# Kernel tuning notes

Hardware: AMD Instinct MI355X
Metric: run time of the kernel (lower is better)

The kernel has to match this reference:

```python
import jax, jax.numpy as jnp
import numpy as np

EMBED_DIM = 256
NUM_HEADS = 4
HEAD_DIM = EMBED_DIM // NUM_HEADS  # 64
FEAT_X = FEAT_Y = 64               # 64*64 = 4096 tokens
THETA = 10000.0


def _axial_cos_sin(dim, end_x, end_y, theta):
    # compute_axial_cis: dim//4 frequencies per spatial axis, concatenated -> [N, dim//2]
    f = 1.0 / (theta ** (np.arange(0, dim, 4)[: dim // 4].astype(np.float32) / dim))
    t = np.arange(end_x * end_y)
    tx = (t % end_x).astype(np.float32)
    ty = (t // end_x).astype(np.float32)
    ang = np.concatenate([np.outer(tx, f), np.outer(ty, f)], axis=-1)  # [N, dim//2]
    return jnp.asarray(np.cos(ang)), jnp.asarray(np.sin(ang))


def _apply_rope(x, cos, sin):
    # x: [B, H, N, D]; adjacent pairs (x[..., 2i], x[..., 2i+1]) are the complex parts
    xr = x.reshape(*x.shape[:-1], -1, 2)
    xa, xb = xr[..., 0], xr[..., 1]          # [B, H, N, D//2]
    oa = xa * cos - xb * sin                  # cos/sin: [N, D//2], broadcast
    ob = xa * sin + xb * cos
    return jnp.stack([oa, ob], axis=-1).reshape(x.shape)


def setup_inputs() -> dict:
    key = jax.random.key(0)
    ks = jax.random.split(key, 8)
    B, N, D = 1, FEAT_X * FEAT_Y, EMBED_DIM
    s = 0.02  # weight init scale
    return {
        "q": jax.random.normal(ks[0], (B, N, D), jnp.float32),
        "k": jax.random.normal(ks[1], (B, N, D), jnp.float32),
        "v": jax.random.normal(ks[2], (B, N, D), jnp.float32),
        "wq": jax.random.normal(ks[3], (D, D), jnp.float32) * s,
        "bq": jnp.zeros((D,), jnp.float32),
        "wk": jax.random.normal(ks[4], (D, D), jnp.float32) * s,
        "bk": jnp.zeros((D,), jnp.float32),
        "wv": jax.random.normal(ks[5], (D, D), jnp.float32) * s,
        "bv": jnp.zeros((D,), jnp.float32),
        "wo": jax.random.normal(ks[6], (D, D), jnp.float32) * s,
        "bo": jnp.zeros((D,), jnp.float32),
        "return_attn": 0,
        "num_k_exclude_rope": 0,
    }


def reference(q, k, v, wq, bq, wk, bk, wv, bv, wo, bo, return_attn, num_k_exclude_rope):
    B, Nq, D = q.shape
    H, hd = NUM_HEADS, HEAD_DIM
    # QKV projections (weights stored [in, out], equiv to torch Linear W.T)
    qp = (q @ wq + bq).reshape(B, Nq, H, hd).transpose(0, 2, 1, 3)   # [B,H,Nq,hd]
    kp = (k @ wk + bk).reshape(B, -1, H, hd).transpose(0, 2, 1, 3)   # [B,H,Nk,hd]
    vp = (v @ wv + bv).reshape(B, -1, H, hd).transpose(0, 2, 1, 3)
    # rotary encoding on q and the first (Nk - num_k_exclude_rope) keys
    cos, sin = _axial_cos_sin(hd, FEAT_X, FEAT_Y, THETA)
    qp = _apply_rope(qp, cos, sin)
    nkr = kp.shape[2] - num_k_exclude_rope  # static Python int
    if num_k_exclude_rope > 0:
        kp = jnp.concatenate([_apply_rope(kp[:, :, :nkr], cos, sin), kp[:, :, nkr:]], axis=2)
    else:
        kp = _apply_rope(kp, cos, sin)
    # SDPA (eval: dropout_p = 0)
    scale = 1.0 / jnp.sqrt(jnp.asarray(hd, qp.dtype))
    scores = jnp.einsum("bhqd,bhkd->bhqk", qp, kp) * scale
    attn = jax.nn.softmax(scores, axis=-1)
    out = jnp.einsum("bhqk,bhkd->bhqd", attn, vp)
    out = out.transpose(0, 2, 1, 3).reshape(B, Nq, D)
    out = out @ wo + bo
    if return_attn:
        return out, scores  # attn_weight = q @ k^T * scale (pre-softmax, as in source)
    return out
```

## Files before the change

kernel.cpp:

```cpp
#include <hip/hip_runtime.h>
#include <hip/hip_bf16.h>
#include <math.h>

#define NTOK 4096
#define DEMB 256
#define NHEAD 4
#define HD 64

typedef short bf16x8 __attribute__((ext_vector_type(8)));
typedef short bf16x4 __attribute__((ext_vector_type(4)));
typedef float f32x4 __attribute__((ext_vector_type(4)));

__device__ __forceinline__ unsigned short f2b(float f) {
  union { float f; unsigned u; } v; v.f = f;
  return (unsigned short)((v.u + 0x7FFFu + ((v.u >> 16) & 1u)) >> 16);
}
__device__ __forceinline__ unsigned packrp(float lo, float hi) {
  return __builtin_amdgcn_perm(__float_as_uint(hi) + 0x8000u,
                               __float_as_uint(lo) + 0x8000u, 0x07060302u);
}

__global__ void prep_kernel(const float* wq, const float* wk, const float* wv,
                            const float* wo, unsigned short* wt, float2* cs) {
  int b = blockIdx.x;
  if (b < 1024) {
    int idx = b * 256 + threadIdx.x;
    int m = idx >> 16, rest = idx & 0xFFFF;
    int o = rest >> 8, i = rest & 255;
    const float* w = (m == 0) ? wq : (m == 1) ? wk : (m == 2) ? wv : wo;
    wt[idx] = f2b(w[i * 256 + o]);
  } else {
    int idx = (b - 1024) * 256 + threadIdx.x;
    int n = idx >> 5, p = idx & 31;
    int j = p & 15;
    float f = powf(10000.0f, -(float)j / 16.0f);
    float ang = ((p < 16) ? (float)(n & 63) : (float)(n >> 6)) * f;
    cs[idx] = make_float2(cosf(ang), sinf(ang));
  }
}

__global__ __launch_bounds__(256) void qkvproj_kernel(
    const float* q, const float* k, const float* v, const unsigned short* wt,
    const float* bq, const float* bk, const float* bv, const float2* cs,
    unsigned short* qp, unsigned short* kp, unsigned short* vt) {
  int which = blockIdx.z;
  int wave = threadIdx.x >> 6, lane = threadIdx.x & 63;
  int col = lane & 15, g = lane >> 4;
  int mbase = blockIdx.x * 64 + wave * 16;
  int nbase = blockIdx.y * 64;
  const float* X = (which == 0) ? q : (which == 1) ? k : v;
  const unsigned short* W = wt + which * 65536;
  const float* bias = (which == 0) ? bq : (which == 1) ? bk : bv;

  f32x4 acc[4] = {};
  const float* ap0 = X + (mbase + col) * 256 + g * 8;
#pragma unroll
  for (int ks = 0; ks < 256; ks += 32) {
    float4 a0 = *(const float4*)(ap0 + ks);
    float4 a1 = *(const float4*)(ap0 + ks + 4);
    bf16x8 af;
    af[0] = (short)f2b(a0.x); af[1] = (short)f2b(a0.y);
    af[2] = (short)f2b(a0.z); af[3] = (short)f2b(a0.w);
    af[4] = (short)f2b(a1.x); af[5] = (short)f2b(a1.y);
    af[6] = (short)f2b(a1.z); af[7] = (short)f2b(a1.w);
#pragma unroll
    for (int nt = 0; nt < 4; ++nt) {
      bf16x8 bf_ = *(const bf16x8*)(W + (nbase + nt * 16 + col) * 256 + ks + g * 8);
      acc[nt] = __builtin_amdgcn_mfma_f32_16x16x32_bf16(af, bf_, acc[nt], 0, 0, 0);
    }
  }

  if (which == 2) {
    int kpos = ((mbase >> 5) << 5) + 8 * g + 4 * ((mbase >> 4) & 1);
#pragma unroll
    for (int nt = 0; nt < 4; ++nt) {
      int c = nbase + nt * 16 + col;
      float b = bias[c];
      bf16x4 pk;
#pragma unroll
      for (int r = 0; r < 4; ++r) pk[r] = (short)f2b(acc[nt][r] + b);
      *(bf16x4*)(vt + c * NTOK + kpos) = pk;
    }
  } else {
    const float QSC = 0.18033688f;
    unsigned short* dst = (which == 0) ? qp : kp;
#pragma unroll
    for (int nt = 0; nt < 4; ++nt) {
      int c = nbase + nt * 16 + col;
      float b = bias[c];
#pragma unroll
      for (int r = 0; r < 4; ++r) {
        int t = mbase + g * 4 + r;
        float val = acc[nt][r] + b;
        float2 csv = cs[t * 32 + ((c & 63) >> 1)];
        float pv = __shfl_xor(val, 1);
        float sn = (c & 1) ? csv.y : -csv.y;
        val = val * csv.x + pv * sn;
        if (which == 0) val *= QSC;
        dst[((c >> 6) * NTOK + t) * HD + (c & 63)] = f2b(val);
      }
    }
  }
}

__global__ __launch_bounds__(512, 4) void attn_kernel(
    const unsigned short* qp, const unsigned short* kp,
    const unsigned short* vt, float* pO, float* pml) {
  __shared__ alignas(16) unsigned char lds[32768];
  int id = blockIdx.x;
  int xcd = id & 7;
  int head = xcd >> 1;
  int rest = id >> 3;
  int qtile = rest >> 2;
  int ks = (xcd & 1) * 4 + (rest & 3);
  int qb = qtile * 128;
  int slot = (head * 32 + qtile) * 8 + ks;
  int w = threadIdx.x >> 6, lane = threadIdx.x & 63;
  int col = lane & 15, g = lane >> 4;
  int stok = threadIdx.x >> 3, spart = threadIdx.x & 7;
  unsigned soff = (unsigned)(stok * 128) +
                  (unsigned)((spart * 16) ^ ((stok & 7) << 4));

  const unsigned short* kgp = kp + (head * NTOK + ks * 512) * HD;
  const unsigned short* vgp = vt + head * HD * NTOK + ks * 512;

  bf16x8 skr, svr;
  auto stage_issue = [&](int t) {
    skr = *(const bf16x8*)(kgp + (t * 64 + stok) * HD + spart * 8);
    svr = *(const bf16x8*)(vgp + stok * NTOK + t * 64 + spart * 8);
  };
  auto stage_write = [&](int buf) {
    *(bf16x8*)(lds + (unsigned)buf * 16384u + soff) = skr;
    *(bf16x8*)(lds + (unsigned)buf * 16384u + 8192u + soff) = svr;
  };

  bf16x8 ones;
#pragma unroll
  for (int i = 0; i < 8; ++i) ones[i] = (short)0x3F80;

  bf16x8 qf[2];
  {
    const unsigned short* qr = qp + (head * NTOK + qb + w * 16) * HD;
#pragma unroll
    for (int h2 = 0; h2 < 2; ++h2)
      qf[h2] = *(const bf16x8*)(qr + col * HD + h2 * 32 + g * 8);
  }

  stage_issue(0);
  stage_write(0);
  stage_issue(1);
  __syncthreads();

  f32x4 acco[4] = {};
  f32x4 lacc = {};
  float mrow = -1e30f;

  for (int t = 0; t < 8; ++t) {
    int cur = t & 1;
    if (t < 7) {
      stage_write(cur ^ 1);
      if (t < 6) stage_issue(t + 2);
    }
    unsigned kb = (unsigned)cur * 16384u, vb = (unsigned)cur * 16384u + 8192u;

    f32x4 st[4] = {};
#pragma unroll
    for (int mt = 0; mt < 4; ++mt) {
      int tok = mt * 16 + col;
      unsigned ro = kb + (unsigned)(tok * 128) + (unsigned)((g * 16) ^ ((tok & 7) << 4));
      bf16x8 kf0 = *(const bf16x8*)(lds + ro);
      bf16x8 kf1 = *(const bf16x8*)(lds + (ro ^ 64u));
      st[mt] = __builtin_amdgcn_mfma_f32_16x16x32_bf16(kf0, qf[0], st[mt], 0, 0, 0);
      st[mt] = __builtin_amdgcn_mfma_f32_16x16x32_bf16(kf1, qf[1], st[mt], 0, 0, 0);
    }

    float pm = fmaxf(fmaxf(st[0][0], st[0][1]), fmaxf(st[0][2], st[0][3]));
#pragma unroll
    for (int mt = 1; mt < 4; ++mt)
      pm = fmaxf(pm, fmaxf(fmaxf(st[mt][0], st[mt][1]), fmaxf(st[mt][2], st[mt][3])));
    if (!__all(pm <= mrow + 8.0f)) {
      float nm = fmaxf(pm, __shfl_xor(pm, 16));
      nm = fmaxf(nm, __shfl_xor(nm, 32));
      nm = fmaxf(nm, mrow);
      float fac = exp2f(mrow - nm);
      mrow = nm;
      float fr0 = __shfl(fac, g * 4 + 0), fr1 = __shfl(fac, g * 4 + 1);
      float fr2 = __shfl(fac, g * 4 + 2), fr3 = __shfl(fac, g * 4 + 3);
#pragma unroll
      for (int nt = 0; nt < 4; ++nt) {
        acco[nt][0] *= fr0; acco[nt][1] *= fr1;
        acco[nt][2] *= fr2; acco[nt][3] *= fr3;
      }
      lacc[0] *= fr0; lacc[1] *= fr1; lacc[2] *= fr2; lacc[3] *= fr3;
    }

    float p[4][4];
#pragma unroll
    for (int mt = 0; mt < 4; ++mt)
#pragma unroll
      for (int r = 0; r < 4; ++r) p[mt][r] = exp2f(st[mt][r] - mrow);
    unsigned pw[2][4];
#pragma unroll
    for (int kk = 0; kk < 2; ++kk) {
      pw[kk][0] = packrp(p[2 * kk][0], p[2 * kk][1]);
      pw[kk][1] = packrp(p[2 * kk][2], p[2 * kk][3]);
      pw[kk][2] = packrp(p[2 * kk + 1][0], p[2 * kk + 1][1]);
      pw[kk][3] = packrp(p[2 * kk + 1][2], p[2 * kk + 1][3]);
    }

#pragma unroll
    for (int kk = 0; kk < 2; ++kk) {
      union { unsigned u[4]; bf16x8 v; } pf;
      pf.u[0] = pw[kk][0]; pf.u[1] = pw[kk][1];
      pf.u[2] = pw[kk][2]; pf.u[3] = pw[kk][3];
      lacc = __builtin_amdgcn_mfma_f32_16x16x32_bf16(pf.v, ones, lacc, 0, 0, 0);
#pragma unroll
      for (int nt = 0; nt < 4; ++nt) {
        int d = nt * 16 + col;
        unsigned off = vb + (unsigned)(d * 128) +
                       (unsigned)((kk * 64 + g * 16) ^ ((d & 7) << 4));
        bf16x8 vf = *(const bf16x8*)(lds + off);
        acco[nt] = __builtin_amdgcn_mfma_f32_16x16x32_bf16(pf.v, vf, acco[nt], 0, 0, 0);
      }
    }
    __syncthreads();
  }

#pragma unroll
  for (int nt = 0; nt < 4; ++nt)
#pragma unroll
    for (int r = 0; r < 4; ++r)
      pO[slot * 8192 + (w * 16 + g * 4 + r) * 64 + nt * 16 + col] = acco[nt][r];
  if (col == 0) {
#pragma unroll
    for (int r = 0; r < 4; ++r)
      pml[slot * 256 + (w * 16 + g * 4 + r) * 2 + 1] = lacc[r];
  }
  if (g == 0)
    pml[slot * 256 + (w * 16 + col) * 2 + 0] = mrow;
}

__global__ __launch_bounds__(256) void merge_kernel(
    const float* pO, const float* pml, unsigned short* att) {
  int bid = blockIdx.x;
  int group = bid >> 1, half = bid & 1;
  int head = group >> 5, qtile = group & 31;
  int t = threadIdx.x;
  int qloc = half * 64 + (t >> 2);
  int d0 = (t & 3) * 16;
  const float* mlb = pml + group * 8 * 256 + qloc * 2;
  float mx = -1e30f;
#pragma unroll
  for (int ks = 0; ks < 8; ++ks) mx = fmaxf(mx, mlb[ks * 256]);
  float den = 0.f, num[16] = {};
#pragma unroll
  for (int ks = 0; ks < 8; ++ks) {
    float wgt = exp2f(mlb[ks * 256] - mx);
    den += wgt * mlb[ks * 256 + 1];
    const float* ob = pO + (group * 8 + ks) * 8192 + qloc * 64 + d0;
#pragma unroll
    for (int i = 0; i < 16; ++i) num[i] += wgt * ob[i];
  }
  float inv = 1.0f / den;
  union { unsigned short s[16]; bf16x8 v[2]; } ov;
#pragma unroll
  for (int i = 0; i < 16; ++i) ov.s[i] = f2b(num[i] * inv);
  unsigned short* dst = att + (qtile * 128 + qloc) * DEMB + head * HD + d0;
  *(bf16x8*)dst = ov.v[0];
  *(bf16x8*)(dst + 8) = ov.v[1];
}

__global__ __launch_bounds__(256) void outproj_kernel(
    const unsigned short* att, const unsigned short* wt_o, const float* bo,
    float* out) {
  int wave = threadIdx.x >> 6, lane = threadIdx.x & 63;
  int col = lane & 15, g = lane >> 4;
  int mbase = blockIdx.x * 64 + wave * 16;
  int nbase = blockIdx.y * 64;
  f32x4 acc[4] = {};
#pragma unroll
  for (int ks = 0; ks < 256; ks += 32) {
    bf16x8 af = *(const bf16x8*)(att + (mbase + col) * 256 + ks + g * 8);
#pragma unroll
    for (int nt = 0; nt < 4; ++nt) {
      bf16x8 bf_ = *(const bf16x8*)(wt_o + (nbase + nt * 16 + col) * 256 + ks + g * 8);
      acc[nt] = __builtin_amdgcn_mfma_f32_16x16x32_bf16(af, bf_, acc[nt], 0, 0, 0);
    }
  }
#pragma unroll
  for (int nt = 0; nt < 4; ++nt) {
    int c = nbase + nt * 16 + col;
    float b = bo[c];
#pragma unroll
    for (int r = 0; r < 4; ++r)
      out[(mbase + g * 4 + r) * 256 + c] = acc[nt][r] + b;
  }
}

extern "C" void kernel_launch(void* const* d_in, const int* in_sizes, int n_in,
                              void* d_out, int out_size, void* d_ws, size_t ws_size,
                              hipStream_t stream) {
  const float* q  = (const float*)d_in[0];
  const float* k  = (const float*)d_in[1];
  const float* v  = (const float*)d_in[2];
  const float* wq = (const float*)d_in[3];
  const float* bq = (const float*)d_in[4];
  const float* wk = (const float*)d_in[5];
  const float* bk = (const float*)d_in[6];
  const float* wv = (const float*)d_in[7];
  const float* bv = (const float*)d_in[8];
  const float* wo = (const float*)d_in[9];
  const float* bo = (const float*)d_in[10];
  float* out = (float*)d_out;

  char* ws = (char*)d_ws;
  float2* cs         = (float2*)ws;
  unsigned short* wt = (unsigned short*)(ws + (1u << 20));
  unsigned short* qp = (unsigned short*)(ws + 1536u * 1024u);
  unsigned short* kp = qp + NHEAD * NTOK * HD;
  unsigned short* vt = kp + NHEAD * NTOK * HD;
  unsigned short* att = vt + NHEAD * NTOK * HD;
  float* pO  = (float*)(ws + 9728u * 1024u);
  float* pml = (float*)(ws + 43008u * 1024u);

  prep_kernel<<<1536, 256, 0, stream>>>(wq, wk, wv, wo, wt, cs);
  qkvproj_kernel<<<dim3(64, 4, 3), 256, 0, stream>>>(q, k, v, wt, bq, bk, bv, cs,
                                                     qp, kp, vt);
  attn_kernel<<<1024, 512, 0, stream>>>(qp, kp, vt, pO, pml);
  merge_kernel<<<256, 256, 0, stream>>>(pO, pml, att);
  outproj_kernel<<<dim3(64, 4), 256, 0, stream>>>(att, wt + 3 * 65536, bo, out);
}
```

Measured before the change: 82.72 us.

## Process two 16-row query subtiles per wave to reuse K/V LDS fragments

Each wave now handles 32 query rows instead of 16, so every K and V fragment read from LDS feeds two MFMAs, halving LDS traffic per unit of work. The attention grid drops to 512 blocks with 256-query tiles, and the merge kernel and partial-buffer indexing are updated to match. The next-tile LDS write and global prefetch now come after the QK^T MFMAs instead of before. Costs are higher register pressure, which may hurt occupancy under launch_bounds(512,4), and fewer blocks to fill the CUs.

```diff
diff --git a/kernel.cpp b/kernel.cpp
--- a/kernel.cpp
+++ b/kernel.cpp
@@ -113,8 +113,8 @@
   int rest = id >> 3;
   int qtile = rest >> 2;
   int ks = (xcd & 1) * 4 + (rest & 3);
-  int qb = qtile * 128;
-  int slot = (head * 32 + qtile) * 8 + ks;
+  int qb = qtile * 256;
+  int slot = (head * 16 + qtile) * 8 + ks;
   int w = threadIdx.x >> 6, lane = threadIdx.x & 63;
   int col = lane & 15, g = lane >> 4;
   int stok = threadIdx.x >> 3, spart = threadIdx.x & 7;
@@ -138,12 +138,14 @@
 #pragma unroll
   for (int i = 0; i < 8; ++i) ones[i] = (short)0x3F80;
 
-  bf16x8 qf[2];
+  bf16x8 qf[2][2];
   {
-    const unsigned short* qr = qp + (head * NTOK + qb + w * 16) * HD;
-#pragma unroll
-    for (int h2 = 0; h2 < 2; ++h2)
-      qf[h2] = *(const bf16x8*)(qr + col * HD + h2 * 32 + g * 8);
+    const unsigned short* qr = qp + (head * NTOK + qb + w * 32) * HD;
+#pragma unroll
+    for (int qt = 0; qt < 2; ++qt)
+#pragma unroll
+      for (int h2 = 0; h2 < 2; ++h2)
+        qf[qt][h2] = *(const bf16x8*)(qr + (qt * 16 + col) * HD + h2 * 32 + g * 8);
   }
 
   stage_issue(0);
@@ -151,76 +153,99 @@
   stage_issue(1);
   __syncthreads();
 
-  f32x4 acco[4] = {};
-  f32x4 lacc = {};
-  float mrow = -1e30f;
+  f32x4 acco[4][2] = {};
+  f32x4 lacc[2] = {};
+  float mrow[2] = {-1e30f, -1e30f};
 
   for (int t = 0; t < 8; ++t) {
     int cur = t & 1;
-    if (t < 7) {
-      stage_write(cur ^ 1);
-      if (t < 6) stage_issue(t + 2);
-    }
     unsigned kb = (unsigned)cur * 16384u, vb = (unsigned)cur * 16384u + 8192u;
 
-    f32x4 st[4] = {};
+    f32x4 st[4][2] = {};
 #pragma unroll
     for (int mt = 0; mt < 4; ++mt) {
       int tok = mt * 16 + col;
       unsigned ro = kb + (unsigned)(tok * 128) + (unsigned)((g * 16) ^ ((tok & 7) << 4));
       bf16x8 kf0 = *(const bf16x8*)(lds + ro);
       bf16x8 kf1 = *(const bf16x8*)(lds + (ro ^ 64u));
-      st[mt] = __builtin_amdgcn_mfma_f32_16x16x32_bf16(kf0, qf[0], st[mt], 0, 0, 0);
-      st[mt] = __builtin_amdgcn_mfma_f32_16x16x32_bf16(kf1, qf[1], st[mt], 0, 0, 0);
-    }
-
-    float pm = fmaxf(fmaxf(st[0][0], st[0][1]), fmaxf(st[0][2], st[0][3]));
-#pragma unroll
-    for (int mt = 1; mt < 4; ++mt)
-      pm = fmaxf(pm, fmaxf(fmaxf(st[mt][0], st[mt][1]), fmaxf(st[mt][2], st[mt][3])));
-    if (!__all(pm <= mrow + 8.0f)) {
-      float nm = fmaxf(pm, __shfl_xor(pm, 16));
-      nm = fmaxf(nm, __shfl_xor(nm, 32));
-      nm = fmaxf(nm, mrow);
-      float fac = exp2f(mrow - nm);
-      mrow = nm;
-      float fr0 = __shfl(fac, g * 4 + 0), fr1 = __shfl(fac, g * 4 + 1);
-      float fr2 = __shfl(fac, g * 4 + 2), fr3 = __shfl(fac, g * 4 + 3);
-#pragma unroll
-      for (int nt = 0; nt < 4; ++nt) {
-        acco[nt][0] *= fr0; acco[nt][1] *= fr1;
-        acco[nt][2] *= fr2; acco[nt][3] *= fr3;
-      }
-      lacc[0] *= fr0; lacc[1] *= fr1; lacc[2] *= fr2; lacc[3] *= fr3;
-    }
-
-    float p[4][4];
-#pragma unroll
-    for (int mt = 0; mt < 4; ++mt)
-#pragma unroll
-      for (int r = 0; r < 4; ++r) p[mt][r] = exp2f(st[mt][r] - mrow);
-    unsigned pw[2][4];
+#pragma unroll
+      for (int qt = 0; qt < 2; ++qt) {
+        st[mt][qt] = __builtin_amdgcn_mfma_f32_16x16x32_bf16(kf0, qf[qt][0], st[mt][qt], 0, 0, 0);
+        st[mt][qt] = __builtin_amdgcn_mfma_f32_16x16x32_bf16(kf1, qf[qt][1], st[mt][qt], 0, 0, 0);
+      }
+    }
+
+    if (t < 7) {
+      stage_write(cur ^ 1);
+      if (t < 6) stage_issue(t + 2);
+    }
+
+    float pm[2];
+#pragma unroll
+    for (int qt = 0; qt < 2; ++qt) {
+      float x = fmaxf(fmaxf(st[0][qt][0], st[0][qt][1]),
+                      fmaxf(st[0][qt][2], st[0][qt][3]));
+#pragma unroll
+      for (int mt = 1; mt < 4; ++mt)
+        x = fmaxf(x, fmaxf(fmaxf(st[mt][qt][0], st[mt][qt][1]),
+                           fmaxf(st[mt][qt][2], st[mt][qt][3])));
+      pm[qt] = x;
+    }
+    if (!__all(pm[0] <= mrow[0] + 8.0f && pm[1] <= mrow[1] + 8.0f)) {
+#pragma unroll
+      for (int qt = 0; qt < 2; ++qt) {
+        float nm = fmaxf(pm[qt], __shfl_xor(pm[qt], 16));
+        nm = fmaxf(nm, __shfl_xor(nm, 32));
+        nm = fmaxf(nm, mrow[qt]);
+        float fac = exp2f(mrow[qt] - nm);
+        mrow[qt] = nm;
+        float fr0 = __shfl(fac, g * 4 + 0), fr1 = __shfl(fac, g * 4 + 1);
+        float fr2 = __shfl(fac, g * 4 + 2), fr3 = __shfl(fac, g * 4 + 3);
+#pragma unroll
+        for (int nt = 0; nt < 4; ++nt) {
+          acco[nt][qt][0] *= fr0; acco[nt][qt][1] *= fr1;
+          acco[nt][qt][2] *= fr2; acco[nt][qt][3] *= fr3;
+        }
+        lacc[qt][0] *= fr0; lacc[qt][1] *= fr1;
+        lacc[qt][2] *= fr2; lacc[qt][3] *= fr3;
+      }
+    }
+
+    unsigned pw[2][2][4];
+#pragma unroll
+    for (int qt = 0; qt < 2; ++qt) {
+      float p[4][4];
+#pragma unroll
+      for (int mt = 0; mt < 4; ++mt)
+#pragma unroll
+        for (int r = 0; r < 4; ++r) p[mt][r] = exp2f(st[mt][qt][r] - mrow[qt]);
+#pragma unroll
+      for (int kk = 0; kk < 2; ++kk) {
+        pw[qt][kk][0] = packrp(p[2 * kk][0], p[2 * kk][1]);
+        pw[qt][kk][1] = packrp(p[2 * kk][2], p[2 * kk][3]);
+        pw[qt][kk][2] = packrp(p[2 * kk + 1][0], p[2 * kk + 1][1]);
+        pw[qt][kk][3] = packrp(p[2 * kk + 1][2], p[2 * kk + 1][3]);
+      }
+    }
+
 #pragma unroll
     for (int kk = 0; kk < 2; ++kk) {
-      pw[kk][0] = packrp(p[2 * kk][0], p[2 * kk][1]);
-      pw[kk][1] = packrp(p[2 * kk][2], p[2 * kk][3]);
-      pw[kk][2] = packrp(p[2 * kk + 1][0], p[2 * kk + 1][1]);
-      pw[kk][3] = packrp(p[2 * kk + 1][2], p[2 * kk + 1][3]);
-    }
-
-#pragma unroll
-    for (int kk = 0; kk < 2; ++kk) {
-      union { unsigned u[4]; bf16x8 v; } pf;
-      pf.u[0] = pw[kk][0]; pf.u[1] = pw[kk][1];
-      pf.u[2] = pw[kk][2]; pf.u[3] = pw[kk][3];
-      lacc = __builtin_amdgcn_mfma_f32_16x16x32_bf16(pf.v, ones, lacc, 0, 0, 0);
+      union { unsigned u[4]; bf16x8 v; } pf[2];
+#pragma unroll
+      for (int qt = 0; qt < 2; ++qt) {
+        pf[qt].u[0] = pw[qt][kk][0]; pf[qt].u[1] = pw[qt][kk][1];
+        pf[qt].u[2] = pw[qt][kk][2]; pf[qt].u[3] = pw[qt][kk][3];
+        lacc[qt] = __builtin_amdgcn_mfma_f32_16x16x32_bf16(pf[qt].v, ones, lacc[qt], 0, 0, 0);
+      }
 #pragma unroll
       for (int nt = 0; nt < 4; ++nt) {
         int d = nt * 16 + col;
         unsigned off = vb + (unsigned)(d * 128) +
                        (unsigned)((kk * 64 + g * 16) ^ ((d & 7) << 4));
         bf16x8 vf = *(const bf16x8*)(lds + off);
-        acco[nt] = __builtin_amdgcn_mfma_f32_16x16x32_bf16(pf.v, vf, acco[nt], 0, 0, 0);
+#pragma unroll
+        for (int qt = 0; qt < 2; ++qt)
+          acco[nt][qt] = __builtin_amdgcn_mfma_f32_16x16x32_bf16(pf[qt].v, vf, acco[nt][qt], 0, 0, 0);
       }
     }
     __syncthreads();
@@ -229,35 +254,43 @@
 #pragma unroll
   for (int nt = 0; nt < 4; ++nt)
 #pragma unroll
-    for (int r = 0; r < 4; ++r)
-      pO[slot * 8192 + (w * 16 + g * 4 + r) * 64 + nt * 16 + col] = acco[nt][r];
+    for (int qt = 0; qt < 2; ++qt)
+#pragma unroll
+      for (int r = 0; r < 4; ++r)
+        pO[slot * 16384 + (w * 32 + qt * 16 + g * 4 + r) * 64 + nt * 16 + col] =
+            acco[nt][qt][r];
   if (col == 0) {
 #pragma unroll
-    for (int r = 0; r < 4; ++r)
-      pml[slot * 256 + (w * 16 + g * 4 + r) * 2 + 1] = lacc[r];
-  }
-  if (g == 0)
-    pml[slot * 256 + (w * 16 + col) * 2 + 0] = mrow;
+    for (int qt = 0; qt < 2; ++qt)
+#pragma unroll
+      for (int r = 0; r < 4; ++r)
+        pml[slot * 512 + (w * 32 + qt * 16 + g * 4 + r) * 2 + 1] = lacc[qt][r];
+  }
+  if (g == 0) {
+#pragma unroll
+    for (int qt = 0; qt < 2; ++qt)
+      pml[slot * 512 + (w * 32 + qt * 16 + col) * 2 + 0] = mrow[qt];
+  }
 }
 
 __global__ __launch_bounds__(256) void merge_kernel(
     const float* pO, const float* pml, unsigned short* att) {
   int bid = blockIdx.x;
-  int group = bid >> 1, half = bid & 1;
-  int head = group >> 5, qtile = group & 31;
+  int group = bid >> 2, quarter = bid & 3;
+  int head = group >> 4, qtile = group & 15;
   int t = threadIdx.x;
-  int qloc = half * 64 + (t >> 2);
+  int qloc = quarter * 64 + (t >> 2);
   int d0 = (t & 3) * 16;
-  const float* mlb = pml + group * 8 * 256 + qloc * 2;
+  const float* mlb = pml + group * 8 * 512 + qloc * 2;
   float mx = -1e30f;
 #pragma unroll
-  for (int ks = 0; ks < 8; ++ks) mx = fmaxf(mx, mlb[ks * 256]);
+  for (int ks = 0; ks < 8; ++ks) mx = fmaxf(mx, mlb[ks * 512]);
   float den = 0.f, num[16] = {};
 #pragma unroll
   for (int ks = 0; ks < 8; ++ks) {
-    float wgt = exp2f(mlb[ks * 256] - mx);
-    den += wgt * mlb[ks * 256 + 1];
-    const float* ob = pO + (group * 8 + ks) * 8192 + qloc * 64 + d0;
+    float wgt = exp2f(mlb[ks * 512] - mx);
+    den += wgt * mlb[ks * 512 + 1];
+    const float* ob = pO + (group * 8 + ks) * 16384 + qloc * 64 + d0;
 #pragma unroll
     for (int i = 0; i < 16; ++i) num[i] += wgt * ob[i];
   }
@@ -265,7 +298,7 @@
   union { unsigned short s[16]; bf16x8 v[2]; } ov;
 #pragma unroll
   for (int i = 0; i < 16; ++i) ov.s[i] = f2b(num[i] * inv);
-  unsigned short* dst = att + (qtile * 128 + qloc) * DEMB + head * HD + d0;
+  unsigned short* dst = att + (qtile * 256 + qloc) * DEMB + head * HD + d0;
   *(bf16x8*)dst = ov.v[0];
   *(bf16x8*)(dst + 8) = ov.v[1];
 }
@@ -326,7 +359,7 @@
   prep_kernel<<<1536, 256, 0, stream>>>(wq, wk, wv, wo, wt, cs);
   qkvproj_kernel<<<dim3(64, 4, 3), 256, 0, stream>>>(q, k, v, wt, bq, bk, bv, cs,
                                                      qp, kp, vt);
-  attn_kernel<<<1024, 512, 0, stream>>>(qp, kp, vt, pO, pml);
+  attn_kernel<<<512, 512, 0, stream>>>(qp, kp, vt, pO, pml);
   merge_kernel<<<256, 256, 0, stream>>>(pO, pml, att);
   outproj_kernel<<<dim3(64, 4), 256, 0, stream>>>(att, wt + 3 * 65536, bo, out);
 }
```

After: 81.96 us. Within noise of the previous version (-0.9%).
